# Performance work log

Hardware: AMD Instinct MI355X
Metric: run time of the kernel (lower is better)

The kernel has to match this reference:

```python
import jax, jax.numpy as jnp
import numpy as np

NUM_CHARTS = 16
LATENT_DIM = 128
RANK = 128
BATCH = 131072


def _init_weight(key, out_dim, in_dim):
    # nn.init.eye_ on top-left block, then += 0.01 * randn (identity-ish init)
    w = jnp.zeros((out_dim, in_dim), jnp.float32)
    m = min(out_dim, in_dim)
    w = w.at[jnp.arange(m), jnp.arange(m)].set(1.0)
    return w + 0.01 * jax.random.normal(key, (out_dim, in_dim), jnp.float32)


def setup_inputs() -> dict:
    key = jax.random.key(0)
    ks = jax.random.split(key, 3 + 2 * NUM_CHARTS)
    z_n = jax.random.normal(ks[0], (BATCH, LATENT_DIM), jnp.float32)
    source_idx = jax.random.randint(ks[1], (BATCH,), 0, NUM_CHARTS, dtype=jnp.int64 if jax.config.jax_enable_x64 else jnp.int32)
    target_idx = jax.random.randint(ks[2], (BATCH,), 0, NUM_CHARTS, dtype=source_idx.dtype)
    # encoder weights: [C, R, D] (torch Linear weight layout [out, in])
    enc_w = jnp.stack([_init_weight(ks[3 + i], RANK, LATENT_DIM) for i in range(NUM_CHARTS)])
    # decoder weights: [C, D, R]
    dec_w = jnp.stack([_init_weight(ks[3 + NUM_CHARTS + i], LATENT_DIM, RANK) for i in range(NUM_CHARTS)])
    c_param = jnp.zeros((NUM_CHARTS, RANK), jnp.float32)
    d_param = jnp.zeros((NUM_CHARTS, LATENT_DIM), jnp.float32)
    return {"z_n": z_n, "source_idx": source_idx, "target_idx": target_idx,
            "enc_w": enc_w, "dec_w": dec_w, "c_param": c_param, "d_param": d_param}


def _apply_per_chart(x, chart_idx, weights):
    # x: [B, in], weights: [C, out, in] -> [B, out]
    # Loop over the small fixed chart count; each chart does one dense GEMM,
    # results routed by mask-select (same math as gather/compute/scatter).
    C = weights.shape[0]
    out = jnp.zeros((x.shape[0], weights.shape[1]), x.dtype)
    for c in range(C):
        yc = x @ weights[c].T  # [B, out]
        out = jnp.where((chart_idx == c)[:, None], yc, out)
    return out


def reference(z_n, source_idx, target_idx, enc_w, dec_w, c_param, d_param):
    # lift_to_global: per-chart encode + bias c[src]
    h = _apply_per_chart(z_n, source_idx, enc_w) + c_param[source_idx]  # [B, R]
    # project_from_global: per-chart decode + bias d[tgt]
    z_out = _apply_per_chart(h, target_idx, dec_w) + d_param[target_idx]  # [B, D]
    return z_out
```

## Files before the change

kernel.cpp:

```cpp
#include <hip/hip_runtime.h>
#include <hip/hip_bf16.h>

#define NB     131072
#define NCH    16
#define NPAIR  256
#define LDW    136
#define LDH    136
#define LDO    132

#define WS_HIST   0
#define WS_OFF    256
#define WS_SORTED 528
#define WS_BYTES  ((WS_SORTED + NB) * 4)

typedef short short8 __attribute__((ext_vector_type(8)));
typedef float f32x4  __attribute__((ext_vector_type(4)));

__device__ __forceinline__ short bfbits(float x) {
    union { __hip_bfloat16 h; short s; } u;
    u.h = __float2bfloat16(x);
    return u.s;
}

__device__ __forceinline__ short8 cvt_frag(const float* __restrict__ p) {
    const f32x4 lo = *(const f32x4*)p;
    const f32x4 hi = *(const f32x4*)(p + 4);
    short8 r;
    r[0] = bfbits(lo[0]); r[1] = bfbits(lo[1]); r[2] = bfbits(lo[2]); r[3] = bfbits(lo[3]);
    r[4] = bfbits(hi[0]); r[5] = bfbits(hi[1]); r[6] = bfbits(hi[2]); r[7] = bfbits(hi[3]);
    return r;
}

__global__ void k_init(int* __restrict__ hist) {
    hist[threadIdx.x] = 0;
}

__global__ __launch_bounds__(256) void k_hist(const int* __restrict__ si,
                                              const int* __restrict__ ti,
                                              int* __restrict__ hist) {
    __shared__ int sh[NPAIR];
    const int t = threadIdx.x;
    sh[t] = 0;
    __syncthreads();
    const int base = blockIdx.x * 1024 + t;
#pragma unroll
    for (int j = 0; j < 4; ++j) {
        const int i = base + j * 256;
        const int k = (si[i] * NCH + ti[i]) & (NPAIR - 1);
        atomicAdd(&sh[k], 1);
    }
    __syncthreads();
    if (sh[t]) atomicAdd(&hist[t], sh[t]);
}

__global__ __launch_bounds__(256) void k_scan(int* __restrict__ hist,
                                              int* __restrict__ off) {
    __shared__ int s[NPAIR];
    const int t = threadIdx.x;
    const int v = hist[t];
    s[t] = v;
    __syncthreads();
#pragma unroll
    for (int d = 1; d < NPAIR; d <<= 1) {
        const int x = (t >= d) ? s[t - d] : 0;
        __syncthreads();
        s[t] += x;
        __syncthreads();
    }
    off[t + 1] = s[t];
    if (t == 0) off[0] = 0;
    hist[t] = s[t] - v;
}

__global__ __launch_bounds__(256) void k_scatter(const int* __restrict__ si,
                                                 const int* __restrict__ ti,
                                                 int* __restrict__ cursor,
                                                 int* __restrict__ sorted) {
    __shared__ int sh[NPAIR];
    __shared__ int sbase[NPAIR];
    const int t = threadIdx.x;
    sh[t] = 0;
    __syncthreads();
    int key[4], rank[4];
    const int base = blockIdx.x * 1024 + t;
#pragma unroll
    for (int j = 0; j < 4; ++j) {
        const int i = base + j * 256;
        const int k = (si[i] * NCH + ti[i]) & (NPAIR - 1);
        key[j]  = k;
        rank[j] = atomicAdd(&sh[k], 1);
    }
    __syncthreads();
    sbase[t] = sh[t] ? atomicAdd(&cursor[t], sh[t]) : 0;
    __syncthreads();
#pragma unroll
    for (int j = 0; j < 4; ++j) {
        const int slot = sbase[key[j]] + rank[j];
        if (slot >= 0 && slot < NB)
            sorted[slot] = base + j * 256;
    }
}

__global__ __launch_bounds__(512, 2)
void k_gemm(const float* __restrict__ z,
            const float* __restrict__ encw,
            const float* __restrict__ decw,
            const float* __restrict__ cpar,
            const float* __restrict__ dpar,
            const int* __restrict__ off,
            const int* __restrict__ sorted,
            float* __restrict__ out) {
    __shared__ int sRow[128];
    __shared__ __align__(16) __hip_bfloat16 sW1[128 * LDW];
    __shared__ __align__(16) __hip_bfloat16 sW2[128 * LDW];
    __shared__ __align__(16) float sOut[128 * LDO];
    __hip_bfloat16* const sH = (__hip_bfloat16*)sOut;

    const int bucket = blockIdx.x;
    const int srcc = bucket >> 4;
    const int tgtc = bucket & (NCH - 1);
    const int beg = off[bucket];
    const int end = off[bucket + 1];

    const int tid  = threadIdx.x;
    const int lane = tid & 63;
    const int wv   = tid >> 6;
    const int lr   = lane & 15;
    const int lhi  = lane >> 4;
    const int mb   = wv * 16;

    {
        const float* W1 = encw + srcc * 16384;
        const float* W2 = decw + tgtc * 16384;
#pragma unroll
        for (int it = 0; it < 4; ++it) {
            const int f = (it * 512 + tid) * 8;
            const int row = f >> 7, col = f & 127;
            *(short8*)(sW1 + row * LDW + col) = cvt_frag(W1 + f);
            *(short8*)(sW2 + row * LDW + col) = cvt_frag(W2 + f);
        }
    }
    __syncthreads();

    float cb[8], db[8];
#pragma unroll
    for (int nt = 0; nt < 8; ++nt) {
        cb[nt] = cpar[srcc * 128 + nt * 16 + lr];
        db[nt] = dpar[tgtc * 128 + nt * 16 + lr];
    }

    const int ntile = (end - beg + 127) >> 7;
    for (int tile = 0; tile < ntile; ++tile) {
        const int rbeg = beg + tile * 128;
        __syncthreads();
        if (tid < 128) {
            const int g = rbeg + tid;
            int v = (g < end) ? sorted[g] : -1;
            sRow[tid] = ((unsigned)v < (unsigned)NB) ? v : -1;
        }
        __syncthreads();

        const int r0 = sRow[mb + lr];
        const float* pz0 = z + (long)(r0 < 0 ? 0 : r0) * 128 + lhi * 8;

        f32x4 acc[8];
#pragma unroll
        for (int nt = 0; nt < 8; ++nt) acc[nt] = (f32x4)(0.0f);

#pragma unroll
        for (int k = 0; k < 4; ++k) {
            const short8 a0 = cvt_frag(pz0 + k * 32);
#pragma unroll
            for (int nt = 0; nt < 8; ++nt) {
                const short8 b = *(const short8*)(sW1 + (nt * 16 + lr) * LDW + k * 32 + lhi * 8);
                acc[nt] = __builtin_amdgcn_mfma_f32_16x16x32_bf16(a0, b, acc[nt], 0, 0, 0);
            }
        }

#pragma unroll
        for (int nt = 0; nt < 8; ++nt) {
            const int row = mb + lhi * 4;
            const int col = nt * 16 + lr;
#pragma unroll
            for (int r = 0; r < 4; ++r)
                sH[(row + r) * LDH + col] = __float2bfloat16(acc[nt][r] + cb[nt]);
        }
        __syncthreads();

#pragma unroll
        for (int nt = 0; nt < 8; ++nt) acc[nt] = (f32x4)(0.0f);

#pragma unroll
        for (int k = 0; k < 4; ++k) {
            const short8 a0 = *(const short8*)(sH + (mb + lr) * LDH + k * 32 + lhi * 8);
#pragma unroll
            for (int nt = 0; nt < 8; ++nt) {
                const short8 b = *(const short8*)(sW2 + (nt * 16 + lr) * LDW + k * 32 + lhi * 8);
                acc[nt] = __builtin_amdgcn_mfma_f32_16x16x32_bf16(a0, b, acc[nt], 0, 0, 0);
            }
        }
        __syncthreads();

#pragma unroll
        for (int nt = 0; nt < 8; ++nt) {
            const int row = mb + lhi * 4;
            const int col = nt * 16 + lr;
#pragma unroll
            for (int r = 0; r < 4; ++r)
                sOut[(row + r) * LDO + col] = acc[nt][r] + db[nt];
        }
        __syncthreads();

        {
            const int rr0 = tid >> 5;
            const int c4  = (tid & 31) * 4;
#pragma unroll
            for (int it = 0; it < 8; ++it) {
                const int rr = rr0 + it * 16;
                const int grow = sRow[rr];
                if (grow >= 0)
                    *(f32x4*)(out + (long)grow * 128 + c4) =
                        *(const f32x4*)(sOut + rr * LDO + c4);
            }
        }
    }
}

__global__ __launch_bounds__(256)
void k_fallback(const float* __restrict__ z,
                const int* __restrict__ si, const int* __restrict__ ti,
                const float* __restrict__ ew,
                const float* __restrict__ dw,
                const float* __restrict__ cp,
                const float* __restrict__ dp,
                float* __restrict__ out) {
    __shared__ float sh[4][128];
    const int lane = threadIdx.x & 63, wv = threadIdx.x >> 6;
    for (int row = blockIdx.x * 4 + wv; row < NB; row += (int)gridDim.x * 4) {
        const int sc = si[row] & (NCH - 1), tc = ti[row] & (NCH - 1);
        const float* zr = z + (long)row * 128;
        const float* W1 = ew + sc * 16384;
        float h0 = cp[sc * 128 + lane];
        float h1 = cp[sc * 128 + lane + 64];
        for (int d = 0; d < 128; ++d) {
            const float zv = zr[d];
            h0 += zv * W1[lane * 128 + d];
            h1 += zv * W1[(lane + 64) * 128 + d];
        }
        sh[wv][lane] = h0;
        sh[wv][lane + 64] = h1;
        __syncthreads();
        const float* W2 = dw + tc * 16384;
        float o0 = dp[tc * 128 + lane];
        float o1 = dp[tc * 128 + lane + 64];
        for (int r = 0; r < 128; ++r) {
            const float hv = sh[wv][r];
            o0 += hv * W2[lane * 128 + r];
            o1 += hv * W2[(lane + 64) * 128 + r];
        }
        out[(long)row * 128 + lane] = o0;
        out[(long)row * 128 + lane + 64] = o1;
        __syncthreads();
    }
}

extern "C" void kernel_launch(void* const* d_in, const int* in_sizes, int n_in,
                              void* d_out, int out_size, void* d_ws, size_t ws_size,
                              hipStream_t stream) {
    const float* z  = (const float*)d_in[0];
    const int*   si = (const int*)d_in[1];
    const int*   ti = (const int*)d_in[2];
    const float* ew = (const float*)d_in[3];
    const float* dw = (const float*)d_in[4];
    const float* cp = (const float*)d_in[5];
    const float* dp = (const float*)d_in[6];
    float* out = (float*)d_out;

    if (ws_size >= (size_t)WS_BYTES) {
        int* hist   = (int*)d_ws + WS_HIST;
        int* off    = (int*)d_ws + WS_OFF;
        int* sorted = (int*)d_ws + WS_SORTED;

        k_init<<<1, NPAIR, 0, stream>>>(hist);
        k_hist<<<128, 256, 0, stream>>>(si, ti, hist);
        k_scan<<<1, NPAIR, 0, stream>>>(hist, off);
        k_scatter<<<128, 256, 0, stream>>>(si, ti, hist, sorted);
        k_gemm<<<NPAIR, 512, 0, stream>>>(z, ew, dw, cp, dp, off, sorted, out);
    } else {
        k_fallback<<<1024, 256, 0, stream>>>(z, si, ti, ew, dw, cp, dp, out);
    }
}
```

Measured before the change: 155.7 us.

## Decouple waves into independent 16-row groups with register prefetch of z rows

Each wave now processes its own 16-row groups independently with a per-wave H buffer, removing the block-wide barriers between the two GEMMs and the output staging. Row indices are loaded in chunks of up to 1024 per barrier, and the next group's z rows are prefetched into registers (double buffered) while the current group computes. Outputs are written directly from accumulators as scattered scalar stores instead of through an LDS-staged coalesced f32x4 store, which trades store coalescing and extra register pressure for less synchronization and lower LDS use.

```diff
diff --git a/kernel.cpp b/kernel.cpp
--- a/kernel.cpp
+++ b/kernel.cpp
@@ -7,6 +7,7 @@
 #define LDW    136
 #define LDH    136
 #define LDO    132
+#define CAP    1024
 
 #define WS_HIST   0
 #define WS_OFF    256
@@ -110,11 +111,10 @@
             const int* __restrict__ off,
             const int* __restrict__ sorted,
             float* __restrict__ out) {
-    __shared__ int sRow[128];
+    __shared__ int sRowLds[CAP];
     __shared__ __align__(16) __hip_bfloat16 sW1[128 * LDW];
     __shared__ __align__(16) __hip_bfloat16 sW2[128 * LDW];
-    __shared__ __align__(16) float sOut[128 * LDO];
-    __hip_bfloat16* const sH = (__hip_bfloat16*)sOut;
+    __shared__ __align__(16) __hip_bfloat16 sH[8 * 16 * LDH];
 
     const int bucket = blockIdx.x;
     const int srcc = bucket >> 4;
@@ -127,7 +127,6 @@
     const int wv   = tid >> 6;
     const int lr   = lane & 15;
     const int lhi  = lane >> 4;
-    const int mb   = wv * 16;
 
     {
         const float* W1 = encw + srcc * 16384;
@@ -140,7 +139,6 @@
             *(short8*)(sW2 + row * LDW + col) = cvt_frag(W2 + f);
         }
     }
-    __syncthreads();
 
     float cb[8], db[8];
 #pragma unroll
@@ -149,79 +147,89 @@
         db[nt] = dpar[tgtc * 128 + nt * 16 + lr];
     }
 
-    const int ntile = (end - beg + 127) >> 7;
-    for (int tile = 0; tile < ntile; ++tile) {
-        const int rbeg = beg + tile * 128;
-        __syncthreads();
-        if (tid < 128) {
-            const int g = rbeg + tid;
-            int v = (g < end) ? sorted[g] : -1;
-            sRow[tid] = ((unsigned)v < (unsigned)NB) ? v : -1;
-        }
-        __syncthreads();
-
-        const int r0 = sRow[mb + lr];
-        const float* pz0 = z + (long)(r0 < 0 ? 0 : r0) * 128 + lhi * 8;
-
+    __hip_bfloat16* const hs = sH + wv * (16 * LDH);
+
+    auto pf = [&](int g, f32x4* buf) {
+        const int rr = sRowLds[(g << 4) + lr];
+        const float* p = z + (long)(rr < 0 ? 0 : rr) * 128 + lhi * 8;
+#pragma unroll
+        for (int k = 0; k < 4; ++k) {
+            buf[2 * k]     = *(const f32x4*)(p + k * 32);
+            buf[2 * k + 1] = *(const f32x4*)(p + k * 32 + 4);
+        }
+    };
+
+    auto do_group = [&](int g, const f32x4* buf) {
         f32x4 acc[8];
 #pragma unroll
         for (int nt = 0; nt < 8; ++nt) acc[nt] = (f32x4)(0.0f);
 
 #pragma unroll
         for (int k = 0; k < 4; ++k) {
-            const short8 a0 = cvt_frag(pz0 + k * 32);
+            const f32x4 lo = buf[2 * k], hi = buf[2 * k + 1];
+            short8 a;
+            a[0] = bfbits(lo[0]); a[1] = bfbits(lo[1]); a[2] = bfbits(lo[2]); a[3] = bfbits(lo[3]);
+            a[4] = bfbits(hi[0]); a[5] = bfbits(hi[1]); a[6] = bfbits(hi[2]); a[7] = bfbits(hi[3]);
 #pragma unroll
             for (int nt = 0; nt < 8; ++nt) {
                 const short8 b = *(const short8*)(sW1 + (nt * 16 + lr) * LDW + k * 32 + lhi * 8);
-                acc[nt] = __builtin_amdgcn_mfma_f32_16x16x32_bf16(a0, b, acc[nt], 0, 0, 0);
+                acc[nt] = __builtin_amdgcn_mfma_f32_16x16x32_bf16(a, b, acc[nt], 0, 0, 0);
             }
         }
 
 #pragma unroll
-        for (int nt = 0; nt < 8; ++nt) {
-            const int row = mb + lhi * 4;
-            const int col = nt * 16 + lr;
+        for (int nt = 0; nt < 8; ++nt)
 #pragma unroll
             for (int r = 0; r < 4; ++r)
-                sH[(row + r) * LDH + col] = __float2bfloat16(acc[nt][r] + cb[nt]);
-        }
-        __syncthreads();
+                hs[(lhi * 4 + r) * LDH + nt * 16 + lr] = __float2bfloat16(acc[nt][r] + cb[nt]);
 
 #pragma unroll
         for (int nt = 0; nt < 8; ++nt) acc[nt] = (f32x4)(0.0f);
 
 #pragma unroll
         for (int k = 0; k < 4; ++k) {
-            const short8 a0 = *(const short8*)(sH + (mb + lr) * LDH + k * 32 + lhi * 8);
+            const short8 a = *(const short8*)(hs + lr * LDH + k * 32 + lhi * 8);
 #pragma unroll
             for (int nt = 0; nt < 8; ++nt) {
                 const short8 b = *(const short8*)(sW2 + (nt * 16 + lr) * LDW + k * 32 + lhi * 8);
-                acc[nt] = __builtin_amdgcn_mfma_f32_16x16x32_bf16(a0, b, acc[nt], 0, 0, 0);
+                acc[nt] = __builtin_amdgcn_mfma_f32_16x16x32_bf16(a, b, acc[nt], 0, 0, 0);
             }
         }
-        __syncthreads();
-
-#pragma unroll
-        for (int nt = 0; nt < 8; ++nt) {
-            const int row = mb + lhi * 4;
-            const int col = nt * 16 + lr;
+
+        int grow[4];
+#pragma unroll
+        for (int r = 0; r < 4; ++r) grow[r] = sRowLds[(g << 4) + lhi * 4 + r];
+#pragma unroll
+        for (int nt = 0; nt < 8; ++nt)
 #pragma unroll
             for (int r = 0; r < 4; ++r)
-                sOut[(row + r) * LDO + col] = acc[nt][r] + db[nt];
-        }
-        __syncthreads();
-
-        {
-            const int rr0 = tid >> 5;
-            const int c4  = (tid & 31) * 4;
-#pragma unroll
-            for (int it = 0; it < 8; ++it) {
-                const int rr = rr0 + it * 16;
-                const int grow = sRow[rr];
-                if (grow >= 0)
-                    *(f32x4*)(out + (long)grow * 128 + c4) =
-                        *(const f32x4*)(sOut + rr * LDO + c4);
-            }
+                if (grow[r] >= 0)
+                    out[(long)grow[r] * 128 + nt * 16 + lr] = acc[nt][r] + db[nt];
+    };
+
+    for (int cb0 = beg; cb0 < end; cb0 += CAP) {
+        const int cnt = min(end - cb0, CAP);
+        __syncthreads();
+        for (int i = tid; i < CAP; i += 512) {
+            int v = (i < cnt) ? sorted[cb0 + i] : -1;
+            sRowLds[i] = ((unsigned)v < (unsigned)NB) ? v : -1;
+        }
+        __syncthreads();
+
+        const int ng = (cnt + 15) >> 4;
+        int g = wv;
+        f32x4 pfA[8], pfB[8];
+        if (g < ng) pf(g, pfA);
+        while (g < ng) {
+            int g1 = g + 8;
+            if (g1 < ng) pf(g1, pfB);
+            do_group(g, pfA);
+            g = g1;
+            if (g >= ng) break;
+            int g2 = g + 8;
+            if (g2 < ng) pf(g2, pfA);
+            do_group(g, pfB);
+            g = g2;
         }
     }
 }
```

Result: faster. 146.9 us (-5.6%).
